# Performance work log

Measured on AMD Instinct MI355X. Metric: run time of the kernel, lower is better.

Reference implementation:

```python
import jax, jax.numpy as jnp
import numpy as np


def setup_inputs() -> dict:
    key = jax.random.key(0)
    k1, k2 = jax.random.split(key)
    B, N, C, H, W = 16, 10000, 3, 32, 32
    x = jax.random.normal(k1, (B, C, H, W), dtype=jnp.float32)
    images = jax.random.normal(k2, (N, C, H, W), dtype=jnp.float32)
    # sval = schedule(t) in (0,1); bt^2 = sval, at = sqrt(1 - sval)
    sval = jnp.asarray(0.5, dtype=jnp.float32)
    return {"x": x, "images": images, "sval": sval}


def reference(x, images, sval):
    # Original math: pwise = x[:,None] - at*images[None]
    #   weights = softmax(-||pwise||^2 / (2 bt^2), over N)
    #   out = -sum_n weights_n * pwise_n / bt^2
    # We decompose ||x - at*img||^2 = ||x||^2 - 2 at x.img + at^2 ||img||^2
    # (GEMM form) and use sum_n w_n (x - at*img_n) = x - at*(w @ imgs),
    # avoiding the [B,N,C,H,W] intermediate. Identical math.
    bt2 = sval                      # bt^2 = schedule(t)
    at = jnp.sqrt(1.0 - sval)       # at = sqrt(1 - schedule(t))
    B = x.shape[0]
    N = images.shape[0]
    xf = x.reshape(B, -1)           # [B, D]
    imf = images.reshape(N, -1)     # [N, D]
    x_sq = jnp.sum(xf * xf, axis=-1)        # [B]
    i_sq = jnp.sum(imf * imf, axis=-1)      # [N]
    cross = xf @ imf.T                      # [B, N]  (main GEMM)
    weight_args = -(x_sq[:, None] - 2.0 * at * cross
                    + (at * at) * i_sq[None, :]) / (2.0 * bt2)
    weights = jax.nn.softmax(weight_args, axis=1)   # [B, N]
    mix = weights @ imf                             # [B, D]
    out = -(xf - at * mix) / bt2                    # [B, D]
    return out.reshape(x.shape)
```

## Files before the change

kernel.cpp:

```cpp
#include <hip/hip_runtime.h>
#include <math.h>

#define BB 16
#define NN 10000
#define DD 3072
#define QQ 12
#define SEL_CUT 40.0f
#define CAP 1024

#define RSTEP2(mm, cc)                                                  \
  {                                                                     \
    const bool up = (lane & (mm)) != 0;                                 \
    _Pragma("unroll")                                                   \
    for (int k = 0; k < (cc); ++k) {                                    \
      float2 lo = accp[k], hi = accp[k + (cc)];                         \
      float sx = up ? lo.x : hi.x, sy = up ? lo.y : hi.y;               \
      float rx = __shfl_xor(sx, (mm), 64);                              \
      float ry = __shfl_xor(sy, (mm), 64);                              \
      accp[k].x = (up ? hi.x : lo.x) + rx;                              \
      accp[k].y = (up ? hi.y : lo.y) + ry;                              \
    }                                                                   \
  }

__global__ __launch_bounds__(256) void k1_partial(
    const float* __restrict__ x, const float* __restrict__ images,
    const float* __restrict__ svalp, float* __restrict__ pd)
{
  const int t = threadIdx.x;
  const int lane = t & 63;
  const int wave = t >> 6;
  const int q = blockIdx.y;
  const int dg = q * 256 + (lane << 2);
  const int n0 = (blockIdx.x * 4 + wave) * 16;

  float4 Arow[16];
#pragma unroll
  for (int r = 0; r < 16; ++r) {
    int nr = n0 + r;
    Arow[r] = *(const float4*)&images[(size_t)(nr < NN ? nr : NN - 1) * DD + dg];
  }

  float4 xr[BB];
#pragma unroll
  for (int b = 0; b < BB; ++b)
    xr[b] = *(const float4*)&x[b * DD + dg];

  const float sval = *svalp;
  const float at = sqrtf(1.f - sval);
  const float k1c = at / sval;
  const float k2c = (1.f - sval) / (2.f * sval);

#pragma unroll
  for (int g = 0; g < 8; ++g) {
    float2 p0 = make_float2(Arow[2 * g].x, Arow[2 * g + 1].x);
    float2 p1 = make_float2(Arow[2 * g].y, Arow[2 * g + 1].y);
    float2 p2 = make_float2(Arow[2 * g].z, Arow[2 * g + 1].z);
    float2 p3 = make_float2(Arow[2 * g].w, Arow[2 * g + 1].w);

    float2 isqp;
    isqp.x = p0.x * p0.x + p1.x * p1.x + p2.x * p2.x + p3.x * p3.x;
    isqp.y = p0.y * p0.y + p1.y * p1.y + p2.y * p2.y + p3.y * p3.y;

    float2 accp[BB];
#pragma unroll
    for (int b = 0; b < BB; ++b) {
      accp[b].x = p0.x * xr[b].x + p1.x * xr[b].y +
                  p2.x * xr[b].z + p3.x * xr[b].w;
      accp[b].y = p0.y * xr[b].x + p1.y * xr[b].y +
                  p2.y * xr[b].z + p3.y * xr[b].w;
    }

    RSTEP2(32, 8)
    RSTEP2(16, 4)
    RSTEP2(8, 2)
    RSTEP2(4, 1)
    accp[0].x += __shfl_xor(accp[0].x, 2, 64);
    accp[0].y += __shfl_xor(accp[0].y, 2, 64);
    accp[0].x += __shfl_xor(accp[0].x, 1, 64);
    accp[0].y += __shfl_xor(accp[0].y, 1, 64);

#pragma unroll
    for (int m = 32; m >= 1; m >>= 1) {
      isqp.x += __shfl_xor(isqp.x, m, 64);
      isqp.y += __shfl_xor(isqp.y, m, 64);
    }

    const int r = lane & 1;
    const int bb = (lane >> 2) & 15;
    const int nn = n0 + 2 * g + r;
    float dotv = r ? accp[0].y : accp[0].x;
    float isv  = r ? isqp.y    : isqp.x;
    if ((lane & 2) == 0 && nn < NN)
      pd[((size_t)q * BB + bb) * NN + nn] = k1c * dotv - k2c * isv;
  }
}

__global__ __launch_bounds__(1024) void k2_select(
    const float* __restrict__ pd, int* __restrict__ cnt,
    int* __restrict__ idx, float* __restrict__ wv)
{
  __shared__ float red[16];
  __shared__ float mshared, lshared;
  const int b = blockIdx.x;
  const int t = threadIdx.x;
  const int lane = t & 63, wave = t >> 6;
  if (t == 0) cnt[b] = 0;

  float a[10];
#pragma unroll
  for (int i = 0; i < 10; ++i) {
    int n = t + (i << 10);
    if (n < NN) {
      float s = 0.f;
#pragma unroll
      for (int qq = 0; qq < QQ; ++qq)
        s += pd[((size_t)qq * BB + b) * NN + n];
      a[i] = s;
    } else {
      a[i] = -INFINITY;
    }
  }

  float mx = -INFINITY;
#pragma unroll
  for (int i = 0; i < 10; ++i) mx = fmaxf(mx, a[i]);
#pragma unroll
  for (int m = 32; m >= 1; m >>= 1) mx = fmaxf(mx, __shfl_xor(mx, m, 64));
  if (lane == 0) red[wave] = mx;
  __syncthreads();
  if (wave == 0) {
    float v = (lane < 16) ? red[lane] : -INFINITY;
#pragma unroll
    for (int m = 8; m >= 1; m >>= 1) v = fmaxf(v, __shfl_xor(v, m, 64));
    if (lane == 0) mshared = v;
  }
  __syncthreads();
  mx = mshared;

  float s = 0.f;
#pragma unroll
  for (int i = 0; i < 10; ++i) s += __expf(a[i] - mx);
#pragma unroll
  for (int m = 32; m >= 1; m >>= 1) s += __shfl_xor(s, m, 64);
  if (lane == 0) red[wave] = s;
  __syncthreads();
  if (wave == 0) {
    float v = (lane < 16) ? red[lane] : 0.f;
#pragma unroll
    for (int m = 8; m >= 1; m >>= 1) v += __shfl_xor(v, m, 64);
    if (lane == 0) lshared = v;
  }
  __syncthreads();
  const float invl = 1.f / lshared;

#pragma unroll
  for (int i = 0; i < 10; ++i) {
    if (a[i] > mx - SEL_CUT) {
      int k = atomicAdd(&cnt[b], 1);
      if (k < CAP) {
        idx[b * CAP + k] = t + (i << 10);
        wv[b * CAP + k] = __expf(a[i] - mx) * invl;
      }
    }
  }
}

__global__ __launch_bounds__(256) void k3_sparse(
    const float* __restrict__ images, const float* __restrict__ x,
    const float* __restrict__ svalp, const int* __restrict__ cnt,
    const int* __restrict__ idx, const float* __restrict__ wv,
    float* __restrict__ out)
{
  const int b = blockIdx.y;
  const int d0 = blockIdx.x * 1024 + (threadIdx.x << 2);
  int c = cnt[b];
  if (c > CAP) c = CAP;

  float4 acc = make_float4(0.f, 0.f, 0.f, 0.f);
  for (int j = 0; j < c; ++j) {
    int n = idx[b * CAP + j];
    float w = wv[b * CAP + j];
    float4 im = *(const float4*)&images[(size_t)n * DD + d0];
    acc.x += w * im.x; acc.y += w * im.y;
    acc.z += w * im.z; acc.w += w * im.w;
  }

  const float sval = *svalp;
  const float at = sqrtf(1.f - sval);
  const float inv_bt2 = 1.f / sval;
  float4 xv = *(const float4*)&x[b * DD + d0];
  float4 o;
  o.x = (at * acc.x - xv.x) * inv_bt2;
  o.y = (at * acc.y - xv.y) * inv_bt2;
  o.z = (at * acc.z - xv.z) * inv_bt2;
  o.w = (at * acc.w - xv.w) * inv_bt2;
  *(float4*)&out[b * DD + d0] = o;
}

extern "C" void kernel_launch(void* const* d_in, const int* in_sizes, int n_in,
                              void* d_out, int out_size, void* d_ws, size_t ws_size,
                              hipStream_t stream) {
  const float* x      = (const float*)d_in[0];
  const float* images = (const float*)d_in[1];
  const float* sval   = (const float*)d_in[2];
  float* out = (float*)d_out;
  float* ws  = (float*)d_ws;

  float* pd  = ws;
  int*   cnt = (int*)(ws + 1920000);
  int*   idx = (int*)(ws + 1920032);
  float* wv  = ws + 1936416;

  hipLaunchKernelGGL(k1_partial, dim3(157, QQ), dim3(256), 0, stream,
                     x, images, sval, pd);
  hipLaunchKernelGGL(k2_select, dim3(16), dim3(1024), 0, stream,
                     pd, cnt, idx, wv);
  hipLaunchKernelGGL(k3_sparse, dim3(3, 16), dim3(256), 0, stream,
                     images, x, sval, cnt, idx, wv, out);
}
```

Before: 216.7 us.

## Accumulate full-D dot products per wave, dropping split-D partial sums

```diff
diff --git a/kernel.cpp b/kernel.cpp
--- a/kernel.cpp
+++ b/kernel.cpp
@@ -4,99 +4,116 @@
 #define BB 16
 #define NN 10000
 #define DD 3072
-#define QQ 12
 #define SEL_CUT 40.0f
 #define CAP 1024
 
-#define RSTEP2(mm, cc)                                                  \
+#define RSTEP2(arr, mm, cc)                                             \
   {                                                                     \
     const bool up = (lane & (mm)) != 0;                                 \
     _Pragma("unroll")                                                   \
     for (int k = 0; k < (cc); ++k) {                                    \
-      float2 lo = accp[k], hi = accp[k + (cc)];                         \
+      float2 lo = arr[k], hi = arr[k + (cc)];                           \
       float sx = up ? lo.x : hi.x, sy = up ? lo.y : hi.y;               \
       float rx = __shfl_xor(sx, (mm), 64);                              \
       float ry = __shfl_xor(sy, (mm), 64);                              \
-      accp[k].x = (up ? hi.x : lo.x) + rx;                              \
-      accp[k].y = (up ? hi.y : lo.y) + ry;                              \
+      arr[k].x = (up ? hi.x : lo.x) + rx;                               \
+      arr[k].y = (up ? hi.y : lo.y) + ry;                               \
     }                                                                   \
   }
-
-__global__ __launch_bounds__(256) void k1_partial(
+#define RFULL(arr)                                                      \
+  RSTEP2(arr, 32, 8)                                                    \
+  RSTEP2(arr, 16, 4)                                                    \
+  RSTEP2(arr, 8, 2)                                                     \
+  RSTEP2(arr, 4, 1)                                                     \
+  arr[0].x += __shfl_xor(arr[0].x, 2, 64);                              \
+  arr[0].y += __shfl_xor(arr[0].y, 2, 64);                              \
+  arr[0].x += __shfl_xor(arr[0].x, 1, 64);                              \
+  arr[0].y += __shfl_xor(arr[0].y, 1, 64);
+
+__global__ __launch_bounds__(256) void k1_args(
     const float* __restrict__ x, const float* __restrict__ images,
-    const float* __restrict__ svalp, float* __restrict__ pd)
+    const float* __restrict__ svalp, float* __restrict__ args)
 {
   const int t = threadIdx.x;
   const int lane = t & 63;
   const int wave = t >> 6;
-  const int q = blockIdx.y;
-  const int dg = q * 256 + (lane << 2);
-  const int n0 = (blockIdx.x * 4 + wave) * 16;
-
-  float4 Arow[16];
-#pragma unroll
-  for (int r = 0; r < 16; ++r) {
-    int nr = n0 + r;
-    Arow[r] = *(const float4*)&images[(size_t)(nr < NN ? nr : NN - 1) * DD + dg];
-  }
-
-  float4 xr[BB];
-#pragma unroll
-  for (int b = 0; b < BB; ++b)
-    xr[b] = *(const float4*)&x[b * DD + dg];
+  const int n0 = (blockIdx.x * 4 + wave) * 4;
+  const int dl = lane << 2;
+
+  const float* __restrict__ r0 = images + (size_t)(n0 + 0) * DD;
+  const float* __restrict__ r1 = images + (size_t)(n0 + 1) * DD;
+  const float* __restrict__ r2 = images + (size_t)(n0 + 2) * DD;
+  const float* __restrict__ r3 = images + (size_t)(n0 + 3) * DD;
+
+  float2 acc0[BB], acc1[BB];
+  float2 isq0 = make_float2(0.f, 0.f), isq1 = make_float2(0.f, 0.f);
+#pragma unroll
+  for (int b = 0; b < BB; ++b) {
+    acc0[b] = make_float2(0.f, 0.f);
+    acc1[b] = make_float2(0.f, 0.f);
+  }
+
+  float4 c0 = *(const float4*)&r0[dl];
+  float4 c1 = *(const float4*)&r1[dl];
+  float4 c2 = *(const float4*)&r2[dl];
+  float4 c3 = *(const float4*)&r3[dl];
+
+#pragma unroll 1
+  for (int c = 0; c < 12; ++c) {
+    float4 A0 = c0, A1 = c1, A2 = c2, A3 = c3;
+    if (c != 11) {
+      const int dn = (c + 1) * 256 + dl;
+      c0 = *(const float4*)&r0[dn];
+      c1 = *(const float4*)&r1[dn];
+      c2 = *(const float4*)&r2[dn];
+      c3 = *(const float4*)&r3[dn];
+    }
+
+    isq0.x += A0.x * A0.x + A0.y * A0.y + A0.z * A0.z + A0.w * A0.w;
+    isq0.y += A1.x * A1.x + A1.y * A1.y + A1.z * A1.z + A1.w * A1.w;
+    isq1.x += A2.x * A2.x + A2.y * A2.y + A2.z * A2.z + A2.w * A2.w;
+    isq1.y += A3.x * A3.x + A3.y * A3.y + A3.z * A3.z + A3.w * A3.w;
+
+    const int dg = c * 256 + dl;
+#pragma unroll
+    for (int b = 0; b < BB; ++b) {
+      float4 xv = *(const float4*)&x[b * DD + dg];
+      acc0[b].x += A0.x * xv.x + A0.y * xv.y + A0.z * xv.z + A0.w * xv.w;
+      acc0[b].y += A1.x * xv.x + A1.y * xv.y + A1.z * xv.z + A1.w * xv.w;
+      acc1[b].x += A2.x * xv.x + A2.y * xv.y + A2.z * xv.z + A2.w * xv.w;
+      acc1[b].y += A3.x * xv.x + A3.y * xv.y + A3.z * xv.z + A3.w * xv.w;
+    }
+  }
+
+  RFULL(acc0)
+  RFULL(acc1)
+#pragma unroll
+  for (int m = 32; m >= 1; m >>= 1) {
+    isq0.x += __shfl_xor(isq0.x, m, 64);
+    isq0.y += __shfl_xor(isq0.y, m, 64);
+    isq1.x += __shfl_xor(isq1.x, m, 64);
+    isq1.y += __shfl_xor(isq1.y, m, 64);
+  }
 
   const float sval = *svalp;
   const float at = sqrtf(1.f - sval);
   const float k1c = at / sval;
   const float k2c = (1.f - sval) / (2.f * sval);
 
-#pragma unroll
-  for (int g = 0; g < 8; ++g) {
-    float2 p0 = make_float2(Arow[2 * g].x, Arow[2 * g + 1].x);
-    float2 p1 = make_float2(Arow[2 * g].y, Arow[2 * g + 1].y);
-    float2 p2 = make_float2(Arow[2 * g].z, Arow[2 * g + 1].z);
-    float2 p3 = make_float2(Arow[2 * g].w, Arow[2 * g + 1].w);
-
-    float2 isqp;
-    isqp.x = p0.x * p0.x + p1.x * p1.x + p2.x * p2.x + p3.x * p3.x;
-    isqp.y = p0.y * p0.y + p1.y * p1.y + p2.y * p2.y + p3.y * p3.y;
-
-    float2 accp[BB];
-#pragma unroll
-    for (int b = 0; b < BB; ++b) {
-      accp[b].x = p0.x * xr[b].x + p1.x * xr[b].y +
-                  p2.x * xr[b].z + p3.x * xr[b].w;
-      accp[b].y = p0.y * xr[b].x + p1.y * xr[b].y +
-                  p2.y * xr[b].z + p3.y * xr[b].w;
-    }
-
-    RSTEP2(32, 8)
-    RSTEP2(16, 4)
-    RSTEP2(8, 2)
-    RSTEP2(4, 1)
-    accp[0].x += __shfl_xor(accp[0].x, 2, 64);
-    accp[0].y += __shfl_xor(accp[0].y, 2, 64);
-    accp[0].x += __shfl_xor(accp[0].x, 1, 64);
-    accp[0].y += __shfl_xor(accp[0].y, 1, 64);
-
-#pragma unroll
-    for (int m = 32; m >= 1; m >>= 1) {
-      isqp.x += __shfl_xor(isqp.x, m, 64);
-      isqp.y += __shfl_xor(isqp.y, m, 64);
-    }
-
-    const int r = lane & 1;
-    const int bb = (lane >> 2) & 15;
-    const int nn = n0 + 2 * g + r;
-    float dotv = r ? accp[0].y : accp[0].x;
-    float isv  = r ? isqp.y    : isqp.x;
-    if ((lane & 2) == 0 && nn < NN)
-      pd[((size_t)q * BB + bb) * NN + nn] = k1c * dotv - k2c * isv;
+  const int r = lane & 1;
+  const int bb = (lane >> 2) & 15;
+  if ((lane & 2) == 0) {
+    float d0 = r ? acc0[0].y : acc0[0].x;
+    float s0 = r ? isq0.y    : isq0.x;
+    args[bb * NN + (n0 + r)] = k1c * d0 - k2c * s0;
+    float d1 = r ? acc1[0].y : acc1[0].x;
+    float s1 = r ? isq1.y    : isq1.x;
+    args[bb * NN + (n0 + 2 + r)] = k1c * d1 - k2c * s1;
   }
 }
 
 __global__ __launch_bounds__(1024) void k2_select(
-    const float* __restrict__ pd, int* __restrict__ cnt,
+    const float* __restrict__ args, int* __restrict__ cnt,
     int* __restrict__ idx, float* __restrict__ wv)
 {
   __shared__ float red[16];
@@ -110,15 +127,7 @@
 #pragma unroll
   for (int i = 0; i < 10; ++i) {
     int n = t + (i << 10);
-    if (n < NN) {
-      float s = 0.f;
-#pragma unroll
-      for (int qq = 0; qq < QQ; ++qq)
-        s += pd[((size_t)qq * BB + b) * NN + n];
-      a[i] = s;
-    } else {
-      a[i] = -INFINITY;
-    }
+    a[i] = (n < NN) ? args[b * NN + n] : -INFINITY;
   }
 
   float mx = -INFINITY;
@@ -206,15 +215,15 @@
   float* out = (float*)d_out;
   float* ws  = (float*)d_ws;
 
-  float* pd  = ws;
-  int*   cnt = (int*)(ws + 1920000);
-  int*   idx = (int*)(ws + 1920032);
-  float* wv  = ws + 1936416;
-
-  hipLaunchKernelGGL(k1_partial, dim3(157, QQ), dim3(256), 0, stream,
-                     x, images, sval, pd);
+  float* args = ws;
+  int*   cnt  = (int*)(ws + 160000);
+  int*   idx  = (int*)(ws + 160032);
+  float* wv   = ws + 176416;
+
+  hipLaunchKernelGGL(k1_args, dim3(625), dim3(256), 0, stream,
+                     x, images, sval, args);
   hipLaunchKernelGGL(k2_select, dim3(16), dim3(1024), 0, stream,
-                     pd, cnt, idx, wv);
+                     args, cnt, idx, wv);
   hipLaunchKernelGGL(k3_sparse, dim3(3, 16), dim3(256), 0, stream,
                      images, x, sval, cnt, idx, wv, out);
 }
```

Measured after the change: 268.2 us. +23.8%, slower.
